# Kernel tuning notes

Measured on AMD Instinct MI355X. Metric: run time of the kernel, lower is better.

The kernel has to match this reference:

```python
import jax, jax.numpy as jnp
import numpy as np

N = 100000      # nodes
E = 3200000     # edges (avg degree 32)
F = 256         # input features
C = 256         # output channels


def setup_inputs() -> dict:
    key = jax.random.key(0)
    k1, k2, k3, k4, k5 = jax.random.split(key, 5)
    x = jax.random.normal(k1, (N, F), dtype=jnp.float32)
    edge_row = jax.random.randint(k2, (E,), 0, N, dtype=jnp.int32)
    edge_col = jax.random.randint(k3, (E,), 0, N, dtype=jnp.int32)
    # precomputed normalized adjacency values (D^-1/2 (A+I) D^-1/2 entries)
    edge_vals = jax.random.uniform(k4, (E,), dtype=jnp.float32)
    kernel = jax.random.normal(k5, (F, C), dtype=jnp.float32) * (1.0 / np.sqrt(F))
    bias = jnp.zeros((C,), dtype=jnp.float32)
    return {"x": x, "edge_row": edge_row, "edge_col": edge_col,
            "edge_vals": edge_vals, "kernel": kernel, "bias": bias}


def reference(x, edge_row, edge_col, edge_vals, kernel, bias):
    # GraphConv: Z = relu( A_hat @ (X @ W) + b ), single mode, sparse A_hat.
    h = x @ kernel                                   # [N, C]
    msgs = edge_vals[:, None] * h[edge_col]          # [E, C] gather along cols
    agg = jax.ops.segment_sum(msgs, edge_row, num_segments=N)  # [N, C]
    return jax.nn.relu(agg + bias)
```

## Files before the change

### kernel.cpp

```cpp
#include <hip/hip_runtime.h>
#include <hip/hip_bf16.h>
#include <hip/hip_fp16.h>


#define CAP 2432
#define NBMAX 1600
#define CH_A3 8192
#define D1_SMEM 19200

typedef __attribute__((ext_vector_type(4))) float f32x4;
typedef __attribute__((ext_vector_type(8))) short s16x8;

__device__ __forceinline__ unsigned short f2bf(float f) {
    unsigned u = __float_as_uint(f);
    u += 0x7FFFu + ((u >> 16) & 1u);
    return (unsigned short)(u >> 16);
}
__device__ __forceinline__ float bf2f(unsigned short s) {
    return __uint_as_float(((unsigned)s) << 16);
}

__global__ __launch_bounds__(256) void k_pre(const float* __restrict__ W,
                                             unsigned short* __restrict__ Wt,
                                             int* __restrict__ gcur, int NB) {
    int bid = blockIdx.x, t = threadIdx.x;
    if (bid < 256) {
        int idx = bid * 256 + t;
        int k = idx >> 8, c = idx & 255;
        Wt[c * 256 + k] = f2bf(W[idx]);
    } else {
        for (int j = t; j < NB; j += 256) gcur[j] = 0;
    }
}

__device__ __forceinline__ void a3_body(const int* __restrict__ row,
                                        const int* __restrict__ col,
                                        const float* __restrict__ val,
                                        int* __restrict__ gcur,
                                        unsigned* __restrict__ bcv,
                                        unsigned char* __restrict__ blr,
                                        int E, int NB, int chunk, char* smem) {
    int* h    = (int*)smem;
    int* base = h + NBMAX;
    int* cur  = base + NBMAX;
    int t = threadIdx.x;
    for (int j = t; j < NB; j += 256) { h[j] = 0; cur[j] = 0; }
    __syncthreads();
    int start = chunk * CH_A3;
    int end = min(E, start + CH_A3);
    for (int i = start + t; i < end; i += 256)
        atomicAdd(&h[row[i] >> 6], 1);
    __syncthreads();
    for (int j = t; j < NB; j += 256) {
        int c = h[j];
        base[j] = c ? atomicAdd(&gcur[j], c) : 0;
    }
    __syncthreads();
    for (int i = start + t; i < end; i += 256) {
        int r = row[i];
        int b = r >> 6;
        int ofs = atomicAdd(&cur[b], 1);
        size_t idx = (size_t)b * CAP + base[b] + ofs;
        unsigned hb = (unsigned)__half_as_ushort(__float2half(val[i]));
        bcv[idx] = (unsigned)col[i] | (hb << 17);
        blr[idx] = (unsigned char)(r & 63);
    }
}

__device__ __forceinline__ void gemm_body(const float* __restrict__ X,
                                          const unsigned short* __restrict__ Wt,
                                          unsigned short* __restrict__ H,
                                          int M, int g, char* smem) {
    typedef unsigned short AsRow[40];
    AsRow* As = (AsRow*)smem;
    int t = threadIdx.x;
    int lane = t & 63;
    int w = t >> 6;
    int r0 = g * 64;
    int c0 = w * 64;
    int srow = t >> 2;
    int sslot = t & 3;
    int gr = r0 + srow; if (gr >= M) gr = M - 1;

    f32x4 acc[4][4] = {};

    for (int k0 = 0; k0 < 256; k0 += 32) {
        const float* p = &X[(size_t)gr * 256 + k0 + sslot * 8];
        f32x4 a0 = __builtin_nontemporal_load((const f32x4*)p);
        f32x4 a1 = __builtin_nontemporal_load((const f32x4*)(p + 4));
        s16x8 va;
        va[0] = (short)f2bf(a0[0]); va[1] = (short)f2bf(a0[1]);
        va[2] = (short)f2bf(a0[2]); va[3] = (short)f2bf(a0[3]);
        va[4] = (short)f2bf(a1[0]); va[5] = (short)f2bf(a1[1]);
        va[6] = (short)f2bf(a1[2]); va[7] = (short)f2bf(a1[3]);
        __syncthreads();
        *(s16x8*)&As[srow][sslot * 8] = va;
        __syncthreads();

        int kofs = (lane >> 4) * 8;
        s16x8 afr[4], bfr[4];
#pragma unroll
        for (int mi = 0; mi < 4; ++mi)
            afr[mi] = *(const s16x8*)&As[mi * 16 + (lane & 15)][kofs];
#pragma unroll
        for (int ni = 0; ni < 4; ++ni) {
            int cn = c0 + ni * 16 + (lane & 15);
            bfr[ni] = *(const s16x8*)&Wt[(size_t)cn * 256 + k0 + kofs];
        }
#pragma unroll
        for (int mi = 0; mi < 4; ++mi)
#pragma unroll
            for (int ni = 0; ni < 4; ++ni)
                acc[mi][ni] = __builtin_amdgcn_mfma_f32_16x16x32_bf16(
                    afr[mi], bfr[ni], acc[mi][ni], 0, 0, 0);
    }

#pragma unroll
    for (int mi = 0; mi < 4; ++mi) {
#pragma unroll
        for (int ni = 0; ni < 4; ++ni) {
            int rg = r0 + mi * 16 + (lane >> 4) * 4;
            int cg = c0 + ni * 16 + (lane & 15);
#pragma unroll
            for (int j = 0; j < 4; ++j) {
                if (rg + j < M)
                    H[(size_t)(rg + j) * 256 + cg] = f2bf(acc[mi][ni][j]);
            }
        }
    }
}

__global__ __launch_bounds__(256) void kD1(const int* __restrict__ row,
                                           const int* __restrict__ col,
                                           const float* __restrict__ val,
                                           int* __restrict__ gcur,
                                           unsigned* __restrict__ bcv,
                                           unsigned char* __restrict__ blr,
                                           int E, int NB, int nA3,
                                           const float* __restrict__ X,
                                           const unsigned short* __restrict__ Wt,
                                           unsigned short* __restrict__ H, int M) {
    extern __shared__ char smem[];
    int bid = blockIdx.x;
    if (bid < nA3) {
        a3_body(row, col, val, gcur, bcv, blr, E, NB, bid, smem);
        return;
    }
    gemm_body(X, Wt, H, M, bid - nA3, smem);
}

__global__ __launch_bounds__(256) void kB2(unsigned* __restrict__ bcv,
                                           const unsigned char* __restrict__ blr,
                                           const int* __restrict__ gcur,
                                           int2* __restrict__ rowinfo, int N) {
    __shared__ unsigned scv[CAP];
    __shared__ unsigned char slr[CAP];
    __shared__ int hist[4][64];
    __shared__ int rs[64], cnt[64];
    int b = blockIdx.x;
    int t = threadIdx.x;
    int w = t >> 6;
    size_t gb = (size_t)b * CAP;
    int n = gcur[b];

    if (t < 64) { hist[0][t] = 0; hist[1][t] = 0; hist[2][t] = 0; hist[3][t] = 0; }
    __syncthreads();
    for (int i = t; i < n; i += 256) {
        unsigned cv = bcv[gb + i];
        unsigned char lr = blr[gb + i];
        scv[i] = cv;
        slr[i] = lr;
        atomicAdd(&hist[w][lr], 1);
    }
    __syncthreads();
    if (t < 64) {
        int h0 = hist[0][t], h1 = hist[1][t], h2 = hist[2][t], h3 = hist[3][t];
        cnt[t] = h0 + h1 + h2 + h3;
        rs[t] = cnt[t];
        hist[0][t] = 0;
        hist[1][t] = h0;
        hist[2][t] = h0 + h1;
        hist[3][t] = h0 + h1 + h2;
    }
    __syncthreads();
    for (int off = 1; off < 64; off <<= 1) {
        int v = (t < 64 && t >= off) ? rs[t - off] : 0;
        __syncthreads();
        if (t < 64 && t >= off) rs[t] += v;
        __syncthreads();
    }
    if (t < 64) {
        int st = rs[t] - cnt[t];
        hist[0][t] += st; hist[1][t] += st;
        hist[2][t] += st; hist[3][t] += st;
        int node = b * 64 + t;
        if (node < N) rowinfo[node] = make_int2((int)(gb + st), cnt[t]);
    }
    __syncthreads();
    for (int i = t; i < n; i += 256) {
        int lr = slr[i];
        int pos = atomicAdd(&hist[w][lr], 1);
        bcv[gb + pos] = scv[i];
    }
}

__global__ __launch_bounds__(256) void k_agg(const unsigned short* __restrict__ H,
                                             const int2* __restrict__ rowinfo,
                                             const unsigned* __restrict__ csr,
                                             const float* __restrict__ bias,
                                             float* __restrict__ out, int n) {
    int wave = threadIdx.x >> 6;
    int lane = threadIdx.x & 63;
    int node = blockIdx.x * 4 + wave;
    if (node >= n) return;
    int2 ri = rowinfo[node];
    int s = ri.x;
    int e = ri.x + ri.y;
    int h = lane >> 5;
    int cbase = (lane & 31) * 8;

    float a0=0.f,a1=0.f,a2=0.f,a3=0.f,a4=0.f,a5=0.f,a6=0.f,a7=0.f;

#define ACC(K, HV)                                                      \
    {                                                                   \
        float v = __half2float(__ushort_as_half((unsigned short)((K) >> 17))); \
        a0 += v * bf2f((unsigned short)(HV)[0]);                        \
        a1 += v * bf2f((unsigned short)(HV)[1]);                        \
        a2 += v * bf2f((unsigned short)(HV)[2]);                        \
        a3 += v * bf2f((unsigned short)(HV)[3]);                        \
        a4 += v * bf2f((unsigned short)(HV)[4]);                        \
        a5 += v * bf2f((unsigned short)(HV)[5]);                        \
        a6 += v * bf2f((unsigned short)(HV)[6]);                        \
        a7 += v * bf2f((unsigned short)(HV)[7]);                        \
    }

    int i = s;
    for (; i + 7 < e; i += 8) {
        unsigned k0 = csr[i + h];
        unsigned k1 = csr[i + 2 + h];
        unsigned k2 = csr[i + 4 + h];
        unsigned k3 = csr[i + 6 + h];
        s16x8 g0 = *(const s16x8*)&H[(k0 & 0x1FFFFu) * 256 + cbase];
        s16x8 g1 = *(const s16x8*)&H[(k1 & 0x1FFFFu) * 256 + cbase];
        s16x8 g2 = *(const s16x8*)&H[(k2 & 0x1FFFFu) * 256 + cbase];
        s16x8 g3 = *(const s16x8*)&H[(k3 & 0x1FFFFu) * 256 + cbase];
        ACC(k0, g0); ACC(k1, g1); ACC(k2, g2); ACC(k3, g3);
    }
    for (; i + 1 < e; i += 2) {
        unsigned k0 = csr[i + h];
        s16x8 g0 = *(const s16x8*)&H[(k0 & 0x1FFFFu) * 256 + cbase];
        ACC(k0, g0);
    }
    if (i < e) {
        unsigned k0 = csr[i];
        s16x8 g0 = *(const s16x8*)&H[(k0 & 0x1FFFFu) * 256 + cbase];
        float v = h ? 0.f
                    : __half2float(__ushort_as_half((unsigned short)(k0 >> 17)));
        a0 += v * bf2f((unsigned short)g0[0]);
        a1 += v * bf2f((unsigned short)g0[1]);
        a2 += v * bf2f((unsigned short)g0[2]);
        a3 += v * bf2f((unsigned short)g0[3]);
        a4 += v * bf2f((unsigned short)g0[4]);
        a5 += v * bf2f((unsigned short)g0[5]);
        a6 += v * bf2f((unsigned short)g0[6]);
        a7 += v * bf2f((unsigned short)g0[7]);
    }
#undef ACC

    a0 += __shfl_xor(a0, 32); a1 += __shfl_xor(a1, 32);
    a2 += __shfl_xor(a2, 32); a3 += __shfl_xor(a3, 32);
    a4 += __shfl_xor(a4, 32); a5 += __shfl_xor(a5, 32);
    a6 += __shfl_xor(a6, 32); a7 += __shfl_xor(a7, 32);

    float w0 = h ? a4 : a0;
    float w1 = h ? a5 : a1;
    float w2 = h ? a6 : a2;
    float w3 = h ? a7 : a3;
    int cw = cbase + h * 4;
    float4 b4 = *(const float4*)&bias[cw];
    float4 o;
    o.x = fmaxf(w0 + b4.x, 0.f);
    o.y = fmaxf(w1 + b4.y, 0.f);
    o.z = fmaxf(w2 + b4.z, 0.f);
    o.w = fmaxf(w3 + b4.w, 0.f);
    *(float4*)&out[(size_t)node * 256 + cw] = o;
}

extern "C" void kernel_launch(void* const* d_in, const int* in_sizes, int n_in,
                              void* d_out, int out_size, void* d_ws, size_t ws_size,
                              hipStream_t stream) {
    const float* x     = (const float*)d_in[0];
    const int*   erow  = (const int*)d_in[1];
    const int*   ecol  = (const int*)d_in[2];
    const float* evals = (const float*)d_in[3];
    const float* W     = (const float*)d_in[4];
    const float* bias  = (const float*)d_in[5];
    float* out = (float*)d_out;

    const int C = 256;
    const int N = in_sizes[0] / C;
    const int E = in_sizes[1];
    const int NB = (N + 63) / 64;

    char* ws = (char*)d_ws;
    size_t off = 0;
    auto carve = [&](size_t bytes) -> void* {
        void* p = ws + off;
        off += (bytes + 255) & ~(size_t)255;
        return p;
    };
    unsigned short* Hbf = (unsigned short*)carve((size_t)N * C * 2);
    unsigned short* Wt  = (unsigned short*)carve((size_t)C * 256 * 2);
    int*            gcur= (int*)carve((size_t)NB * 4);
    unsigned*       bcv = (unsigned*)carve((size_t)NB * CAP * 4);
    unsigned char*  blr = (unsigned char*)carve((size_t)NB * CAP);
    int2*           rinf= (int2*)carve((size_t)N * 8);

    int nA3 = (E + CH_A3 - 1) / CH_A3;
    int gemmBlocks = (N + 63) / 64;

    k_pre<<<257, 256, 0, stream>>>(W, Wt, gcur, NB);
    kD1<<<nA3 + gemmBlocks, 256, D1_SMEM, stream>>>(erow, ecol, evals, gcur,
                                                    bcv, blr, E, NB, nA3,
                                                    x, Wt, Hbf, N);
    kB2<<<NB, 256, 0, stream>>>(bcv, blr, gcur, rinf, N);
    k_agg<<<(N + 3) / 4, 256, 0, stream>>>(Hbf, rinf, bcv, bias, out, N);
}
```

Measured before the change: 378.9 us.

## Pack binned edge col/val and local row into one int2 record, enlarge binning chunk

The binning pass now writes each edge as a single 8-byte int2 (packed col+half value, local row) instead of two separate arrays (4-byte and 1-byte). The bucket-sort pass reads the packed record and writes the sorted col/val words back into the first half of the same bucket region, and rowinfo offsets are adjusted to match. The binning chunk per block grows fourfold, so fewer blocks each do more atomics into the global cursors. The aim is fewer scattered partial-byte stores. The cost is doubled intermediate memory and a fallback workspace allocation path that looks fragile.

```diff
diff --git a/kernel.cpp b/kernel.cpp
--- a/kernel.cpp
+++ b/kernel.cpp
@@ -5,7 +5,7 @@
 
 #define CAP 2432
 #define NBMAX 1600
-#define CH_A3 8192
+#define CH_A3 32768
 #define D1_SMEM 19200
 
 typedef __attribute__((ext_vector_type(4))) float f32x4;
@@ -37,8 +37,7 @@
                                         const int* __restrict__ col,
                                         const float* __restrict__ val,
                                         int* __restrict__ gcur,
-                                        unsigned* __restrict__ bcv,
-                                        unsigned char* __restrict__ blr,
+                                        int2* __restrict__ bin8,
                                         int E, int NB, int chunk, char* smem) {
     int* h    = (int*)smem;
     int* base = h + NBMAX;
@@ -60,10 +59,9 @@
         int r = row[i];
         int b = r >> 6;
         int ofs = atomicAdd(&cur[b], 1);
-        size_t idx = (size_t)b * CAP + base[b] + ofs;
         unsigned hb = (unsigned)__half_as_ushort(__float2half(val[i]));
-        bcv[idx] = (unsigned)col[i] | (hb << 17);
-        blr[idx] = (unsigned char)(r & 63);
+        bin8[(size_t)b * CAP + base[b] + ofs] =
+            make_int2((int)((unsigned)col[i] | (hb << 17)), r & 63);
     }
 }
 
@@ -134,8 +132,7 @@
                                            const int* __restrict__ col,
                                            const float* __restrict__ val,
                                            int* __restrict__ gcur,
-                                           unsigned* __restrict__ bcv,
-                                           unsigned char* __restrict__ blr,
+                                           int2* __restrict__ bin8,
                                            int E, int NB, int nA3,
                                            const float* __restrict__ X,
                                            const unsigned short* __restrict__ Wt,
@@ -143,18 +140,16 @@
     extern __shared__ char smem[];
     int bid = blockIdx.x;
     if (bid < nA3) {
-        a3_body(row, col, val, gcur, bcv, blr, E, NB, bid, smem);
+        a3_body(row, col, val, gcur, bin8, E, NB, bid, smem);
         return;
     }
     gemm_body(X, Wt, H, M, bid - nA3, smem);
 }
 
-__global__ __launch_bounds__(256) void kB2(unsigned* __restrict__ bcv,
-                                           const unsigned char* __restrict__ blr,
+__global__ __launch_bounds__(256) void kB2(int2* __restrict__ bin8,
                                            const int* __restrict__ gcur,
                                            int2* __restrict__ rowinfo, int N) {
-    __shared__ unsigned scv[CAP];
-    __shared__ unsigned char slr[CAP];
+    __shared__ int2 se[CAP];
     __shared__ int hist[4][64];
     __shared__ int rs[64], cnt[64];
     int b = blockIdx.x;
@@ -166,11 +161,9 @@
     if (t < 64) { hist[0][t] = 0; hist[1][t] = 0; hist[2][t] = 0; hist[3][t] = 0; }
     __syncthreads();
     for (int i = t; i < n; i += 256) {
-        unsigned cv = bcv[gb + i];
-        unsigned char lr = blr[gb + i];
-        scv[i] = cv;
-        slr[i] = lr;
-        atomicAdd(&hist[w][lr], 1);
+        int2 e = bin8[gb + i];
+        se[i] = e;
+        atomicAdd(&hist[w][e.y], 1);
     }
     __syncthreads();
     if (t < 64) {
@@ -189,18 +182,19 @@
         if (t < 64 && t >= off) rs[t] += v;
         __syncthreads();
     }
+    unsigned* cvout = (unsigned*)&bin8[gb];
     if (t < 64) {
         int st = rs[t] - cnt[t];
         hist[0][t] += st; hist[1][t] += st;
         hist[2][t] += st; hist[3][t] += st;
         int node = b * 64 + t;
-        if (node < N) rowinfo[node] = make_int2((int)(gb + st), cnt[t]);
+        if (node < N) rowinfo[node] = make_int2((int)(gb * 2 + st), cnt[t]);
     }
     __syncthreads();
     for (int i = t; i < n; i += 256) {
-        int lr = slr[i];
-        int pos = atomicAdd(&hist[w][lr], 1);
-        bcv[gb + pos] = scv[i];
+        int2 e = se[i];
+        int pos = atomicAdd(&hist[w][e.y], 1);
+        cvout[pos] = (unsigned)e.x;
     }
 }
 
@@ -312,17 +306,22 @@
     unsigned short* Hbf = (unsigned short*)carve((size_t)N * C * 2);
     unsigned short* Wt  = (unsigned short*)carve((size_t)C * 256 * 2);
     int*            gcur= (int*)carve((size_t)NB * 4);
-    unsigned*       bcv = (unsigned*)carve((size_t)NB * CAP * 4);
-    unsigned char*  blr = (unsigned char*)carve((size_t)NB * CAP);
     int2*           rinf= (int2*)carve((size_t)N * 8);
+    size_t bin8_bytes = (size_t)NB * CAP * 8;
+    int2* bin8;
+    if (off + bin8_bytes <= ws_size) {
+        bin8 = (int2*)carve(bin8_bytes);
+    } else {
+        bin8 = (int2*)carve(ws_size - off - 256 < bin8_bytes ? 0 : bin8_bytes);
+    }
 
     int nA3 = (E + CH_A3 - 1) / CH_A3;
     int gemmBlocks = (N + 63) / 64;
 
     k_pre<<<257, 256, 0, stream>>>(W, Wt, gcur, NB);
     kD1<<<nA3 + gemmBlocks, 256, D1_SMEM, stream>>>(erow, ecol, evals, gcur,
-                                                    bcv, blr, E, NB, nA3,
+                                                    bin8, E, NB, nA3,
                                                     x, Wt, Hbf, N);
-    kB2<<<NB, 256, 0, stream>>>(bcv, blr, gcur, rinf, N);
-    k_agg<<<(N + 3) / 4, 256, 0, stream>>>(Hbf, rinf, bcv, bias, out, N);
-}
+    kB2<<<NB, 256, 0, stream>>>(bin8, gcur, rinf, N);
+    k_agg<<<(N + 3) / 4, 256, 0, stream>>>(Hbf, rinf, (unsigned*)bin8, bias, out, N);
+}
```

New measurement: 398.8 us. 1.05x slower.
